# Kernel optimization log

Measured on AMD Instinct MI355X. Metric: run time of the kernel, lower is better.

Reference implementation:

```python
import jax, jax.numpy as jnp
import numpy as np

B, S, IN_DIM = 2, 2048, 1024
DIMS, QH, KVH = 1024, 16, 4
HD = DIMS // QH          # head_dims = 64
G = QH // KVH            # groups = 4


def setup_inputs() -> dict:
    key = jax.random.key(0)
    k1, k2, k3, k4, k5, k6 = jax.random.split(key, 6)
    scale = 0.02
    q_in = jax.random.normal(k1, (B, S, IN_DIM), dtype=jnp.float32)
    kv_in = jax.random.normal(k2, (B, S, IN_DIM), dtype=jnp.float32)
    # causal mask (True = attend)
    mask = jnp.tril(jnp.ones((S, S), dtype=bool))
    Wq = jax.random.normal(k3, (IN_DIM, QH, HD), dtype=jnp.float32) * scale
    Wk = jax.random.normal(k4, (IN_DIM, KVH, HD), dtype=jnp.float32) * scale
    Wv = jax.random.normal(k5, (IN_DIM, KVH, HD), dtype=jnp.float32) * scale
    Wo = jax.random.normal(k6, (KVH * HD, IN_DIM), dtype=jnp.float32) * scale
    return {"q_in": q_in, "kv_in": kv_in, "mask": mask,
            "Wq": Wq, "Wk": Wk, "Wv": Wv, "Wo": Wo}


def reference(q_in, kv_in, mask, Wq, Wk, Wv, Wo):
    b, s, _ = q_in.shape
    # projections (DenseGeneral, no bias)
    q = jnp.einsum('bsi,ihd->bshd', q_in, Wq)   # [B,S,QH,HD]
    k = jnp.einsum('bsi,ihd->bshd', kv_in, Wk)  # [B,S,KVH,HD]
    v = jnp.einsum('bsi,ihd->bshd', kv_in, Wv)  # [B,S,KVH,HD]
    # rearrange '... s (h g) d -> ... g h s d' with g=G (h outer, g inner),
    # then einsum '... g h s d, ... h a d -> ... h s a' sums over g.
    # Equivalent (and cheaper): sum q over the group axis first.
    q_g = q.reshape(b, s, KVH, G, HD).sum(axis=3)        # [B,S,KVH,HD]
    q_g = jnp.transpose(q_g, (0, 2, 1, 3))               # [B,KVH,S,HD]
    k = jnp.transpose(k, (0, 2, 1, 3))                   # [B,KVH,S,HD]
    v = jnp.transpose(v, (0, 2, 1, 3))                   # [B,KVH,S,HD]
    scores = jnp.einsum('bhsd,bhad->bhsa', q_g, k)       # [B,KVH,S,S]
    scores = jnp.where(mask[None, None, :, :], scores, -jnp.inf)
    attn = jax.nn.softmax(scores / (HD ** 0.5), axis=-1)
    out = jnp.einsum('bhsa,bhad->bhsd', attn, v)         # [B,KVH,S,HD]
    out = jnp.transpose(out, (0, 2, 1, 3)).reshape(b, s, KVH * HD)
    return out @ Wo                                      # [B,S,IN_DIM]
```

## Files before the change

### kernel.cpp

```cpp
#include <hip/hip_runtime.h>
#include <hip/hip_bf16.h>

#define SS 2048

typedef __attribute__((ext_vector_type(8))) short bf16x8;
typedef __attribute__((ext_vector_type(4))) float f32x4;

__device__ __forceinline__ short f2bf(float f){
    unsigned u = __float_as_uint(f);
    u += 0x7fff + ((u >> 16) & 1);
    return (short)(u >> 16);
}

__global__ __launch_bounds__(256) void k_prep_w(const float* __restrict__ Wq,
                                                const float* __restrict__ Wk,
                                                const float* __restrict__ Wv,
                                                const float* __restrict__ Wo,
                                                short* __restrict__ WcatT,
                                                short* __restrict__ WoT){
    __shared__ float Ts[64][65];
    const int bx = blockIdx.x;
    const int r  = threadIdx.x >> 2;
    const int cq = (threadIdx.x & 3) * 16;
    if (bx < 192) {
        const int ktile = bx & 15, ntile = bx >> 4;
        const int k0 = ktile * 64, n0 = ntile * 64;
        if (ntile < 4) {
            const float* base = Wq + (size_t)(k0 + r) * 1024 + ntile * 256;
            #pragma unroll
            for (int i = 0; i < 16; i += 4) {
                float4 a = *(const float4*)(base + cq + i);
                float4 b = *(const float4*)(base + 64 + cq + i);
                float4 c = *(const float4*)(base + 128 + cq + i);
                float4 d = *(const float4*)(base + 192 + cq + i);
                Ts[r][cq+i]   = 0.125f * (a.x + b.x + c.x + d.x);
                Ts[r][cq+i+1] = 0.125f * (a.y + b.y + c.y + d.y);
                Ts[r][cq+i+2] = 0.125f * (a.z + b.z + c.z + d.z);
                Ts[r][cq+i+3] = 0.125f * (a.w + b.w + c.w + d.w);
            }
        } else {
            const float* W = (ntile < 8) ? Wk : Wv;
            const float* base = W + (size_t)(k0 + r) * 256 + (ntile & 3) * 64;
            #pragma unroll
            for (int i = 0; i < 16; i += 4) {
                float4 a = *(const float4*)(base + cq + i);
                Ts[r][cq+i] = a.x; Ts[r][cq+i+1] = a.y;
                Ts[r][cq+i+2] = a.z; Ts[r][cq+i+3] = a.w;
            }
        }
        __syncthreads();
        short tmp[16];
        #pragma unroll
        for (int i = 0; i < 16; ++i) tmp[i] = f2bf(Ts[cq+i][r]);
        short* dst = WcatT + (size_t)(n0 + r) * 1024 + k0 + cq;
        *(bf16x8*)dst       = *(bf16x8*)&tmp[0];
        *(bf16x8*)(dst + 8) = *(bf16x8*)&tmp[8];
    } else {
        const int b2 = bx - 192;
        const int ktile = b2 & 3, ntile = b2 >> 2;
        const int k0 = ktile * 64, n0 = ntile * 64;
        const float* base = Wo + (size_t)(k0 + r) * 1024 + n0;
        #pragma unroll
        for (int i = 0; i < 16; i += 4) {
            float4 a = *(const float4*)(base + cq + i);
            Ts[r][cq+i] = a.x; Ts[r][cq+i+1] = a.y;
            Ts[r][cq+i+2] = a.z; Ts[r][cq+i+3] = a.w;
        }
        __syncthreads();
        short tmp[16];
        #pragma unroll
        for (int i = 0; i < 16; ++i) tmp[i] = f2bf(Ts[cq+i][r]);
        short* dst = WoT + (size_t)(n0 + r) * 256 + k0 + cq;
        *(bf16x8*)dst       = *(bf16x8*)&tmp[0];
        *(bf16x8*)(dst + 8) = *(bf16x8*)&tmp[8];
    }
}

__global__ __launch_bounds__(256) void k_gemm1(const float* __restrict__ q_in,
                                               const float* __restrict__ kv_in,
                                               const short* __restrict__ WcatT,
                                               short* __restrict__ pqk,
                                               short* __restrict__ vt){
    const int m0 = blockIdx.x * 64;
    const int n0 = blockIdx.y * 64;
    const float* X = (n0 < 256) ? q_in : kv_in;
    const int tid = threadIdx.x;
    const int wave = tid >> 6, lane = tid & 63, quad = lane >> 4, l16 = lane & 15;
    const int r = tid >> 2, c = (tid & 3) * 16;

    __shared__ short As[64][72];
    __shared__ short Bs[64][72];

    f32x4 acc[4];
    #pragma unroll
    for (int t = 0; t < 4; ++t) acc[t] = f32x4{0.f, 0.f, 0.f, 0.f};

    for (int k0 = 0; k0 < 1024; k0 += 64) {
        const float* asrc = X + (size_t)(m0 + r) * 1024 + k0 + c;
        short tmp[16];
        #pragma unroll
        for (int i = 0; i < 16; i += 4) {
            float4 f = *(const float4*)(asrc + i);
            tmp[i] = f2bf(f.x); tmp[i+1] = f2bf(f.y);
            tmp[i+2] = f2bf(f.z); tmp[i+3] = f2bf(f.w);
        }
        *(bf16x8*)&As[r][c]     = *(bf16x8*)&tmp[0];
        *(bf16x8*)&As[r][c + 8] = *(bf16x8*)&tmp[8];
        const short* bsrc = WcatT + (size_t)(n0 + r) * 1024 + k0 + c;
        *(bf16x8*)&Bs[r][c]     = *(const bf16x8*)bsrc;
        *(bf16x8*)&Bs[r][c + 8] = *(const bf16x8*)(bsrc + 8);
        __syncthreads();
        #pragma unroll
        for (int ks = 0; ks < 2; ++ks) {
            bf16x8 a = *(bf16x8*)&As[wave * 16 + l16][ks * 32 + quad * 8];
            #pragma unroll
            for (int t = 0; t < 4; ++t) {
                bf16x8 b = *(bf16x8*)&Bs[t * 16 + l16][ks * 32 + quad * 8];
                acc[t] = __builtin_amdgcn_mfma_f32_16x16x32_bf16(a, b, acc[t], 0, 0, 0);
            }
        }
        __syncthreads();
    }
    const int mrow = m0 + wave * 16 + quad * 4;
    if (n0 < 512) {
        #pragma unroll
        for (int t = 0; t < 4; ++t) {
            int col = n0 + t * 16 + l16;
            #pragma unroll
            for (int rg = 0; rg < 4; ++rg)
                pqk[(size_t)(mrow + rg) * 512 + col] = f2bf(acc[t][rg]);
        }
    } else {
        #pragma unroll
        for (int t = 0; t < 4; ++t) {
            int col = n0 - 512 + t * 16 + l16;
            int vh = col >> 6, d = col & 63;
            #pragma unroll
            for (int rg = 0; rg < 4; ++rg) {
                int m = mrow + rg, batch = m >> 11, s = m & 2047;
                vt[((size_t)((batch * 4 + vh) * 64 + d)) * 2048 + s] = f2bf(acc[t][rg]);
            }
        }
    }
}

__global__ __launch_bounds__(256) void k_attn4(const short* __restrict__ pqk,
                                               const short* __restrict__ vt,
                                               float* __restrict__ Op,
                                               float* __restrict__ Lp,
                                               int nsplit){
    const int bx = blockIdx.x;
    const int qt = 31 - (bx / nsplit);
    const int s  = bx - (bx / nsplit) * nsplit;
    const int kv = blockIdx.y, batch = blockIdx.z;
    const int tid = threadIdx.x;
    const int wave = tid >> 6, lane = tid & 63, quad = lane >> 4, l16 = lane & 15;
    const int r = tid >> 2, c = (tid & 3) * 16;
    const int part = (((batch * 4 + kv) * 32 + qt) * nsplit + s);

    __shared__ short Ks[64][72];
    __shared__ short Vs[64][72];
    __shared__ short Ps[64][72];

    const size_t qrow = (size_t)(batch * SS + qt * 64 + wave * 16 + l16);
    bf16x8 aq0 = *(const bf16x8*)(pqk + qrow * 512 + kv * 64 + quad * 8);
    bf16x8 aq1 = *(const bf16x8*)(pqk + qrow * 512 + kv * 64 + 32 + quad * 8);

    f32x4 accO[4];
    #pragma unroll
    for (int t = 0; t < 4; ++t) accO[t] = f32x4{0.f, 0.f, 0.f, 0.f};
    float lrow[4] = {0.f, 0.f, 0.f, 0.f};

    bf16x8 rk0, rk1, rv0, rv1;
    int kt = s;
    if (kt <= qt) {
        const short* ksrc = pqk + (size_t)(batch * SS + kt * 64 + r) * 512 + 256 + kv * 64 + c;
        rk0 = *(const bf16x8*)ksrc; rk1 = *(const bf16x8*)(ksrc + 8);
        const short* vsrc = vt + ((size_t)((batch * 4 + kv) * 64 + r)) * 2048 + kt * 64 + c;
        rv0 = *(const bf16x8*)vsrc; rv1 = *(const bf16x8*)(vsrc + 8);
    }
    for (; kt <= qt; kt += nsplit) {
        *(bf16x8*)&Ks[r][c]     = rk0;
        *(bf16x8*)&Ks[r][c + 8] = rk1;
        *(bf16x8*)&Vs[r][c]     = rv0;
        *(bf16x8*)&Vs[r][c + 8] = rv1;
        __syncthreads();
        if (kt + nsplit <= qt) {
            const short* ksrc = pqk + (size_t)(batch * SS + (kt + nsplit) * 64 + r) * 512 + 256 + kv * 64 + c;
            rk0 = *(const bf16x8*)ksrc; rk1 = *(const bf16x8*)(ksrc + 8);
            const short* vsrc = vt + ((size_t)((batch * 4 + kv) * 64 + r)) * 2048 + (kt + nsplit) * 64 + c;
            rv0 = *(const bf16x8*)vsrc; rv1 = *(const bf16x8*)(vsrc + 8);
        }

        f32x4 sc[4];
        #pragma unroll
        for (int t = 0; t < 4; ++t) sc[t] = f32x4{0.f, 0.f, 0.f, 0.f};
        #pragma unroll
        for (int ks = 0; ks < 2; ++ks) {
            bf16x8 a = ks ? aq1 : aq0;
            #pragma unroll
            for (int t = 0; t < 4; ++t) {
                bf16x8 b = *(bf16x8*)&Ks[t * 16 + l16][ks * 32 + quad * 8];
                sc[t] = __builtin_amdgcn_mfma_f32_16x16x32_bf16(a, b, sc[t], 0, 0, 0);
            }
        }
        if (kt == qt) {
            #pragma unroll
            for (int t = 0; t < 4; ++t) {
                int colg = t * 16 + l16;
                #pragma unroll
                for (int rg = 0; rg < 4; ++rg)
                    if (colg > wave * 16 + quad * 4 + rg) sc[t][rg] = -1e30f;
            }
        }
        #pragma unroll
        for (int t = 0; t < 4; ++t) {
            #pragma unroll
            for (int rg = 0; rg < 4; ++rg) {
                float p = __expf(sc[t][rg]);
                lrow[rg] += p;
                Ps[wave * 16 + quad * 4 + rg][t * 16 + l16] = f2bf(p);
            }
        }
        #pragma unroll
        for (int ks = 0; ks < 2; ++ks) {
            bf16x8 ap = *(bf16x8*)&Ps[wave * 16 + l16][ks * 32 + quad * 8];
            #pragma unroll
            for (int t = 0; t < 4; ++t) {
                bf16x8 bv = *(bf16x8*)&Vs[t * 16 + l16][ks * 32 + quad * 8];
                accO[t] = __builtin_amdgcn_mfma_f32_16x16x32_bf16(ap, bv, accO[t], 0, 0, 0);
            }
        }
        __syncthreads();
    }
    #pragma unroll
    for (int rg = 0; rg < 4; ++rg) {
        float l = lrow[rg];
        l += __shfl_xor(l, 1);
        l += __shfl_xor(l, 2);
        l += __shfl_xor(l, 4);
        l += __shfl_xor(l, 8);
        lrow[rg] = l;
    }
    #pragma unroll
    for (int rg = 0; rg < 4; ++rg) {
        int row = wave * 16 + quad * 4 + rg;
        #pragma unroll
        for (int t = 0; t < 4; ++t)
            Op[(size_t)part * 4096 + row * 64 + t * 16 + l16] = accO[t][rg];
    }
    if (l16 == 0) {
        #pragma unroll
        for (int rg = 0; rg < 4; ++rg)
            Lp[part * 64 + (wave * 16 + quad * 4 + rg)] = lrow[rg];
    }
}

__global__ __launch_bounds__(256) void k_combine(const float* __restrict__ Op,
                                                 const float* __restrict__ Lp,
                                                 short* __restrict__ ao,
                                                 int nsplit){
    const int qt = blockIdx.x, kv = blockIdx.y, batch = blockIdx.z;
    const int tid = threadIdx.x;
    const int rr = tid >> 2, cs = (tid & 3) * 16;
    const int pbase = ((batch * 4 + kv) * 32 + qt) * nsplit;
    float lsum = 0.f;
    for (int i = 0; i < nsplit; ++i) lsum += Lp[(pbase + i) * 64 + rr];
    float inv = 1.f / lsum;
    float o[16];
    #pragma unroll
    for (int j = 0; j < 16; ++j) o[j] = 0.f;
    for (int i = 0; i < nsplit; ++i) {
        const float* src = Op + (size_t)(pbase + i) * 4096 + rr * 64 + cs;
        #pragma unroll
        for (int j = 0; j < 16; j += 4) {
            float4 f = *(const float4*)(src + j);
            o[j] += f.x; o[j+1] += f.y; o[j+2] += f.z; o[j+3] += f.w;
        }
    }
    short* dst = ao + (size_t)(batch * SS + qt * 64 + rr) * 256 + kv * 64 + cs;
    #pragma unroll
    for (int j = 0; j < 16; ++j)
        dst[j] = f2bf(o[j] * inv);
}

__global__ __launch_bounds__(256) void k_gemm2(const short* __restrict__ ao,
                                               const short* __restrict__ WoT,
                                               float* __restrict__ out){
    const int m0 = blockIdx.x * 64;
    const int n0 = blockIdx.y * 64;
    const int tid = threadIdx.x;
    const int wave = tid >> 6, lane = tid & 63, quad = lane >> 4, l16 = lane & 15;
    const int r = tid >> 2, c = (tid & 3) * 16;

    __shared__ short As[64][72];
    __shared__ short Bs[64][72];

    f32x4 acc[4];
    #pragma unroll
    for (int t = 0; t < 4; ++t) acc[t] = f32x4{0.f, 0.f, 0.f, 0.f};

    for (int k0 = 0; k0 < 256; k0 += 64) {
        const short* asrc = ao + (size_t)(m0 + r) * 256 + k0 + c;
        *(bf16x8*)&As[r][c]     = *(const bf16x8*)asrc;
        *(bf16x8*)&As[r][c + 8] = *(const bf16x8*)(asrc + 8);
        const short* bsrc = WoT + (size_t)(n0 + r) * 256 + k0 + c;
        *(bf16x8*)&Bs[r][c]     = *(const bf16x8*)bsrc;
        *(bf16x8*)&Bs[r][c + 8] = *(const bf16x8*)(bsrc + 8);
        __syncthreads();
        #pragma unroll
        for (int ks = 0; ks < 2; ++ks) {
            bf16x8 a = *(bf16x8*)&As[wave * 16 + l16][ks * 32 + quad * 8];
            #pragma unroll
            for (int t = 0; t < 4; ++t) {
                bf16x8 b = *(bf16x8*)&Bs[t * 16 + l16][ks * 32 + quad * 8];
                acc[t] = __builtin_amdgcn_mfma_f32_16x16x32_bf16(a, b, acc[t], 0, 0, 0);
            }
        }
        __syncthreads();
    }
    const int mrow = m0 + wave * 16 + quad * 4;
    #pragma unroll
    for (int t = 0; t < 4; ++t) {
        int col = n0 + t * 16 + l16;
        #pragma unroll
        for (int rg = 0; rg < 4; ++rg)
            out[(size_t)(mrow + rg) * 1024 + col] = acc[t][rg];
    }
}

extern "C" void kernel_launch(void* const* d_in, const int* in_sizes, int n_in,
                              void* d_out, int out_size, void* d_ws, size_t ws_size,
                              hipStream_t stream) {
    const float* q_in  = (const float*)d_in[0];
    const float* kv_in = (const float*)d_in[1];
    int wqi = 3;
    for (int i = 2; i < n_in; ++i)
        if (in_sizes[i] == 1024 * 16 * 64) { wqi = i; break; }
    const float* Wq = (const float*)d_in[wqi];
    const float* Wk = (const float*)d_in[wqi + 1];
    const float* Wv = (const float*)d_in[wqi + 2];
    const float* Wo = (const float*)d_in[wqi + 3];
    float* out = (float*)d_out;

    char* ws = (char*)d_ws;
    char* ob = (char*)d_out;
    short* WcatT = (short*)(ws);
    short* WoT   = (short*)(ws + 1572864);
    short* ao    = (short*)(ws + 2097152);
    short *pqk, *vt; float *Op, *Lp; int nsplit;
    if (ws_size >= (size_t)34 * 1024 * 1024) {
        nsplit = 4;
        pqk = (short*)(ws + 4194304);
        vt  = (short*)(ws + 8388608);
        Lp  = (float*)(ws + 10485760);
        Op  = (float*)(ws + 16777216);
    } else {
        nsplit = 2;
        pqk = (short*)(ob);
        vt  = (short*)(ob + 4194304);
        Op  = (float*)(ob + 6291456);
        Lp  = (float*)(ob + 14680064);
    }

    hipLaunchKernelGGL(k_prep_w,  dim3(256),    dim3(256), 0, stream,
                       Wq, Wk, Wv, Wo, WcatT, WoT);
    hipLaunchKernelGGL(k_gemm1,   dim3(64, 12), dim3(256), 0, stream,
                       q_in, kv_in, WcatT, pqk, vt);
    hipLaunchKernelGGL(k_attn4,   dim3(32 * nsplit, 4, 2), dim3(256), 0, stream,
                       pqk, vt, Op, Lp, nsplit);
    hipLaunchKernelGGL(k_combine, dim3(32, 4, 2), dim3(256), 0, stream,
                       Op, Lp, ao, nsplit);
    hipLaunchKernelGGL(k_gemm2,   dim3(64, 16), dim3(256), 0, stream,
                       ao, WoT, out);
}
```

Baseline: 162.5 us.

## Pre-convert activations to bf16 and use 128x128 GEMM tiles

Adds a separate kernel that converts q_in and kv_in to bf16 once, so the projection GEMM no longer converts fp32 inside its inner loop. Both the projection GEMM and the output GEMM move from 64x64 to 128x128 block tiles, with each wave computing a 4x4 grid of MFMA tiles to improve operand reuse. The workspace layout is fixed to always use nsplit=4 and drops the fallback that placed buffers in the output. In exchange it adds an extra launch and a bf16 copy of the activations, cuts the GEMM grids to far fewer blocks (192 and 256), which may underfill the GPU, and requires a larger workspace.

```diff
diff --git a/kernel.cpp b/kernel.cpp
--- a/kernel.cpp
+++ b/kernel.cpp
@@ -76,69 +76,96 @@
     }
 }
 
-__global__ __launch_bounds__(256) void k_gemm1(const float* __restrict__ q_in,
-                                               const float* __restrict__ kv_in,
+__global__ __launch_bounds__(256) void k_prep_x(const float* __restrict__ q_in,
+                                                const float* __restrict__ kv_in,
+                                                short* __restrict__ xq,
+                                                short* __restrict__ xkv){
+    const float* src = blockIdx.y ? kv_in : q_in;
+    short* dst = blockIdx.y ? xkv : xq;
+    int i = (blockIdx.x * 256 + threadIdx.x) * 4;
+    float4 f = *(const float4*)(src + i);
+    short4 o;
+    o.x = f2bf(f.x); o.y = f2bf(f.y); o.z = f2bf(f.z); o.w = f2bf(f.w);
+    *(short4*)(dst + i) = o;
+}
+
+__global__ __launch_bounds__(256) void k_gemm1(const short* __restrict__ xq,
+                                               const short* __restrict__ xkv,
                                                const short* __restrict__ WcatT,
                                                short* __restrict__ pqk,
                                                short* __restrict__ vt){
-    const int m0 = blockIdx.x * 64;
-    const int n0 = blockIdx.y * 64;
-    const float* X = (n0 < 256) ? q_in : kv_in;
+    const int m0 = blockIdx.x * 128;
+    const int n0 = blockIdx.y * 128;
+    const short* X = (n0 < 256) ? xq : xkv;
     const int tid = threadIdx.x;
     const int wave = tid >> 6, lane = tid & 63, quad = lane >> 4, l16 = lane & 15;
-    const int r = tid >> 2, c = (tid & 3) * 16;
-
-    __shared__ short As[64][72];
-    __shared__ short Bs[64][72];
-
-    f32x4 acc[4];
-    #pragma unroll
-    for (int t = 0; t < 4; ++t) acc[t] = f32x4{0.f, 0.f, 0.f, 0.f};
+    const int wrow = (wave & 1) * 64, wcol = (wave >> 1) * 64;
+    const int r = tid >> 2, cc = (tid & 3) * 16;
+
+    __shared__ short As[128][72];
+    __shared__ short Bs[128][72];
+
+    f32x4 acc[4][4];
+    #pragma unroll
+    for (int tm = 0; tm < 4; ++tm)
+        #pragma unroll
+        for (int tn = 0; tn < 4; ++tn) acc[tm][tn] = f32x4{0.f,0.f,0.f,0.f};
 
     for (int k0 = 0; k0 < 1024; k0 += 64) {
-        const float* asrc = X + (size_t)(m0 + r) * 1024 + k0 + c;
-        short tmp[16];
-        #pragma unroll
-        for (int i = 0; i < 16; i += 4) {
-            float4 f = *(const float4*)(asrc + i);
-            tmp[i] = f2bf(f.x); tmp[i+1] = f2bf(f.y);
-            tmp[i+2] = f2bf(f.z); tmp[i+3] = f2bf(f.w);
-        }
-        *(bf16x8*)&As[r][c]     = *(bf16x8*)&tmp[0];
-        *(bf16x8*)&As[r][c + 8] = *(bf16x8*)&tmp[8];
-        const short* bsrc = WcatT + (size_t)(n0 + r) * 1024 + k0 + c;
-        *(bf16x8*)&Bs[r][c]     = *(const bf16x8*)bsrc;
-        *(bf16x8*)&Bs[r][c + 8] = *(const bf16x8*)(bsrc + 8);
+        const short* a0 = X + (size_t)(m0 + r) * 1024 + k0 + cc;
+        const short* a1 = X + (size_t)(m0 + r + 64) * 1024 + k0 + cc;
+        const short* b0 = WcatT + (size_t)(n0 + r) * 1024 + k0 + cc;
+        const short* b1 = WcatT + (size_t)(n0 + r + 64) * 1024 + k0 + cc;
+        *(bf16x8*)&As[r][cc]          = *(const bf16x8*)a0;
+        *(bf16x8*)&As[r][cc + 8]      = *(const bf16x8*)(a0 + 8);
+        *(bf16x8*)&As[r + 64][cc]     = *(const bf16x8*)a1;
+        *(bf16x8*)&As[r + 64][cc + 8] = *(const bf16x8*)(a1 + 8);
+        *(bf16x8*)&Bs[r][cc]          = *(const bf16x8*)b0;
+        *(bf16x8*)&Bs[r][cc + 8]      = *(const bf16x8*)(b0 + 8);
+        *(bf16x8*)&Bs[r + 64][cc]     = *(const bf16x8*)b1;
+        *(bf16x8*)&Bs[r + 64][cc + 8] = *(const bf16x8*)(b1 + 8);
         __syncthreads();
         #pragma unroll
         for (int ks = 0; ks < 2; ++ks) {
-            bf16x8 a = *(bf16x8*)&As[wave * 16 + l16][ks * 32 + quad * 8];
-            #pragma unroll
-            for (int t = 0; t < 4; ++t) {
-                bf16x8 b = *(bf16x8*)&Bs[t * 16 + l16][ks * 32 + quad * 8];
-                acc[t] = __builtin_amdgcn_mfma_f32_16x16x32_bf16(a, b, acc[t], 0, 0, 0);
-            }
-        }
-        __syncthreads();
-    }
-    const int mrow = m0 + wave * 16 + quad * 4;
+            bf16x8 a[4];
+            #pragma unroll
+            for (int tm = 0; tm < 4; ++tm)
+                a[tm] = *(bf16x8*)&As[wrow + tm * 16 + l16][ks * 32 + quad * 8];
+            #pragma unroll
+            for (int tn = 0; tn < 4; ++tn) {
+                bf16x8 b = *(bf16x8*)&Bs[wcol + tn * 16 + l16][ks * 32 + quad * 8];
+                #pragma unroll
+                for (int tm = 0; tm < 4; ++tm)
+                    acc[tm][tn] = __builtin_amdgcn_mfma_f32_16x16x32_bf16(a[tm], b, acc[tm][tn], 0, 0, 0);
+            }
+        }
+        __syncthreads();
+    }
     if (n0 < 512) {
         #pragma unroll
-        for (int t = 0; t < 4; ++t) {
-            int col = n0 + t * 16 + l16;
-            #pragma unroll
-            for (int rg = 0; rg < 4; ++rg)
-                pqk[(size_t)(mrow + rg) * 512 + col] = f2bf(acc[t][rg]);
+        for (int tm = 0; tm < 4; ++tm) {
+            const int mrow = m0 + wrow + tm * 16 + quad * 4;
+            #pragma unroll
+            for (int tn = 0; tn < 4; ++tn) {
+                const int col = n0 + wcol + tn * 16 + l16;
+                #pragma unroll
+                for (int rg = 0; rg < 4; ++rg)
+                    pqk[(size_t)(mrow + rg) * 512 + col] = f2bf(acc[tm][tn][rg]);
+            }
         }
     } else {
         #pragma unroll
-        for (int t = 0; t < 4; ++t) {
-            int col = n0 - 512 + t * 16 + l16;
-            int vh = col >> 6, d = col & 63;
-            #pragma unroll
-            for (int rg = 0; rg < 4; ++rg) {
-                int m = mrow + rg, batch = m >> 11, s = m & 2047;
-                vt[((size_t)((batch * 4 + vh) * 64 + d)) * 2048 + s] = f2bf(acc[t][rg]);
+        for (int tm = 0; tm < 4; ++tm) {
+            const int mrow = m0 + wrow + tm * 16 + quad * 4;
+            #pragma unroll
+            for (int tn = 0; tn < 4; ++tn) {
+                const int colv = n0 - 512 + wcol + tn * 16 + l16;
+                const int vh = colv >> 6, d = colv & 63;
+                #pragma unroll
+                for (int rg = 0; rg < 4; ++rg) {
+                    int m = mrow + rg, batch = m >> 11, s = m & 2047;
+                    vt[((size_t)((batch * 4 + vh) * 64 + d)) * 2048 + s] = f2bf(acc[tm][tn][rg]);
+                }
             }
         }
     }
@@ -287,45 +314,62 @@
 __global__ __launch_bounds__(256) void k_gemm2(const short* __restrict__ ao,
                                                const short* __restrict__ WoT,
                                                float* __restrict__ out){
-    const int m0 = blockIdx.x * 64;
-    const int n0 = blockIdx.y * 64;
+    const int m0 = blockIdx.x * 128;
+    const int n0 = blockIdx.y * 128;
     const int tid = threadIdx.x;
     const int wave = tid >> 6, lane = tid & 63, quad = lane >> 4, l16 = lane & 15;
-    const int r = tid >> 2, c = (tid & 3) * 16;
-
-    __shared__ short As[64][72];
-    __shared__ short Bs[64][72];
-
-    f32x4 acc[4];
-    #pragma unroll
-    for (int t = 0; t < 4; ++t) acc[t] = f32x4{0.f, 0.f, 0.f, 0.f};
+    const int wrow = (wave & 1) * 64, wcol = (wave >> 1) * 64;
+    const int r = tid >> 2, cc = (tid & 3) * 16;
+
+    __shared__ short As[128][72];
+    __shared__ short Bs[128][72];
+
+    f32x4 acc[4][4];
+    #pragma unroll
+    for (int tm = 0; tm < 4; ++tm)
+        #pragma unroll
+        for (int tn = 0; tn < 4; ++tn) acc[tm][tn] = f32x4{0.f,0.f,0.f,0.f};
 
     for (int k0 = 0; k0 < 256; k0 += 64) {
-        const short* asrc = ao + (size_t)(m0 + r) * 256 + k0 + c;
-        *(bf16x8*)&As[r][c]     = *(const bf16x8*)asrc;
-        *(bf16x8*)&As[r][c + 8] = *(const bf16x8*)(asrc + 8);
-        const short* bsrc = WoT + (size_t)(n0 + r) * 256 + k0 + c;
-        *(bf16x8*)&Bs[r][c]     = *(const bf16x8*)bsrc;
-        *(bf16x8*)&Bs[r][c + 8] = *(const bf16x8*)(bsrc + 8);
+        const short* a0 = ao + (size_t)(m0 + r) * 256 + k0 + cc;
+        const short* a1 = ao + (size_t)(m0 + r + 64) * 256 + k0 + cc;
+        const short* b0 = WoT + (size_t)(n0 + r) * 256 + k0 + cc;
+        const short* b1 = WoT + (size_t)(n0 + r + 64) * 256 + k0 + cc;
+        *(bf16x8*)&As[r][cc]          = *(const bf16x8*)a0;
+        *(bf16x8*)&As[r][cc + 8]      = *(const bf16x8*)(a0 + 8);
+        *(bf16x8*)&As[r + 64][cc]     = *(const bf16x8*)a1;
+        *(bf16x8*)&As[r + 64][cc + 8] = *(const bf16x8*)(a1 + 8);
+        *(bf16x8*)&Bs[r][cc]          = *(const bf16x8*)b0;
+        *(bf16x8*)&Bs[r][cc + 8]      = *(const bf16x8*)(b0 + 8);
+        *(bf16x8*)&Bs[r + 64][cc]     = *(const bf16x8*)b1;
+        *(bf16x8*)&Bs[r + 64][cc + 8] = *(const bf16x8*)(b1 + 8);
         __syncthreads();
         #pragma unroll
         for (int ks = 0; ks < 2; ++ks) {
-            bf16x8 a = *(bf16x8*)&As[wave * 16 + l16][ks * 32 + quad * 8];
-            #pragma unroll
-            for (int t = 0; t < 4; ++t) {
-                bf16x8 b = *(bf16x8*)&Bs[t * 16 + l16][ks * 32 + quad * 8];
-                acc[t] = __builtin_amdgcn_mfma_f32_16x16x32_bf16(a, b, acc[t], 0, 0, 0);
-            }
-        }
-        __syncthreads();
-    }
-    const int mrow = m0 + wave * 16 + quad * 4;
-    #pragma unroll
-    for (int t = 0; t < 4; ++t) {
-        int col = n0 + t * 16 + l16;
-        #pragma unroll
-        for (int rg = 0; rg < 4; ++rg)
-            out[(size_t)(mrow + rg) * 1024 + col] = acc[t][rg];
+            bf16x8 a[4];
+            #pragma unroll
+            for (int tm = 0; tm < 4; ++tm)
+                a[tm] = *(bf16x8*)&As[wrow + tm * 16 + l16][ks * 32 + quad * 8];
+            #pragma unroll
+            for (int tn = 0; tn < 4; ++tn) {
+                bf16x8 b = *(bf16x8*)&Bs[wcol + tn * 16 + l16][ks * 32 + quad * 8];
+                #pragma unroll
+                for (int tm = 0; tm < 4; ++tm)
+                    acc[tm][tn] = __builtin_amdgcn_mfma_f32_16x16x32_bf16(a[tm], b, acc[tm][tn], 0, 0, 0);
+            }
+        }
+        __syncthreads();
+    }
+    #pragma unroll
+    for (int tm = 0; tm < 4; ++tm) {
+        const int mrow = m0 + wrow + tm * 16 + quad * 4;
+        #pragma unroll
+        for (int tn = 0; tn < 4; ++tn) {
+            const int col = n0 + wcol + tn * 16 + l16;
+            #pragma unroll
+            for (int rg = 0; rg < 4; ++rg)
+                out[(size_t)(mrow + rg) * 1024 + col] = acc[tm][tn][rg];
+        }
     }
 }
 
@@ -344,33 +388,27 @@
     float* out = (float*)d_out;
 
     char* ws = (char*)d_ws;
-    char* ob = (char*)d_out;
     short* WcatT = (short*)(ws);
     short* WoT   = (short*)(ws + 1572864);
     short* ao    = (short*)(ws + 2097152);
-    short *pqk, *vt; float *Op, *Lp; int nsplit;
-    if (ws_size >= (size_t)34 * 1024 * 1024) {
-        nsplit = 4;
-        pqk = (short*)(ws + 4194304);
-        vt  = (short*)(ws + 8388608);
-        Lp  = (float*)(ws + 10485760);
-        Op  = (float*)(ws + 16777216);
-    } else {
-        nsplit = 2;
-        pqk = (short*)(ob);
-        vt  = (short*)(ob + 4194304);
-        Op  = (float*)(ob + 6291456);
-        Lp  = (float*)(ob + 14680064);
-    }
-
-    hipLaunchKernelGGL(k_prep_w,  dim3(256),    dim3(256), 0, stream,
+    short* pqk   = (short*)(ws + 4194304);
+    short* vt    = (short*)(ws + 8388608);
+    float* Lp    = (float*)(ws + 10485760);
+    short* xq    = (short*)(ws + 12582912);
+    short* xkv   = (short*)(ws + 20971520);
+    float* Op    = (float*)(ws + 33554432);
+    const int nsplit = 4;
+
+    hipLaunchKernelGGL(k_prep_w,  dim3(256),     dim3(256), 0, stream,
                        Wq, Wk, Wv, Wo, WcatT, WoT);
-    hipLaunchKernelGGL(k_gemm1,   dim3(64, 12), dim3(256), 0, stream,
-                       q_in, kv_in, WcatT, pqk, vt);
+    hipLaunchKernelGGL(k_prep_x,  dim3(4096, 2), dim3(256), 0, stream,
+                       q_in, kv_in, xq, xkv);
+    hipLaunchKernelGGL(k_gemm1,   dim3(32, 6),   dim3(256), 0, stream,
+                       xq, xkv, WcatT, pqk, vt);
     hipLaunchKernelGGL(k_attn4,   dim3(32 * nsplit, 4, 2), dim3(256), 0, stream,
                        pqk, vt, Op, Lp, nsplit);
     hipLaunchKernelGGL(k_combine, dim3(32, 4, 2), dim3(256), 0, stream,
                        Op, Lp, ao, nsplit);
-    hipLaunchKernelGGL(k_gemm2,   dim3(64, 16), dim3(256), 0, stream,
+    hipLaunchKernelGGL(k_gemm2,   dim3(32, 8),   dim3(256), 0, stream,
                        ao, WoT, out);
 }
```

Result: no change. 165.6 us (+1.9%).
